# Kernel optimization log

Measured on AMD Instinct MI355X. Metric: run time of the kernel, lower is better.

The kernel has to match this reference:

```python
import jax, jax.numpy as jnp
import numpy as np

NUM_GRAPHS = 1024


def setup_inputs() -> dict:
    key = jax.random.key(0)
    k1, k2, k3, k4, k5, k6 = jax.random.split(key, 6)
    N, F_DIM, E = 100000, 512, 3200000
    x = jax.random.normal(k1, (N, F_DIM), dtype=jnp.float32)
    edge_index = jax.random.randint(k2, (2, E), 0, N, dtype=jnp.int64)
    edge_attr = jax.random.normal(k3, (E, 7), dtype=jnp.float32)
    batch_size = jnp.sort(jax.random.randint(k4, (N,), 0, NUM_GRAPHS, dtype=jnp.int64))
    W = jax.random.normal(k5, (7, F_DIM), dtype=jnp.float32) * 0.02
    b = jax.random.normal(k6, (7,), dtype=jnp.float32) * 0.02
    return {"x": x, "edge_index": edge_index, "edge_attr": edge_attr,
            "batch_size": batch_size, "W": W, "b": b}


def reference(x, edge_index, edge_attr, batch_size, W, b):
    # Faithful to source forward: conv1/conv2 outputs (h) are discarded by the
    # original code; the returned value depends only on x via mean-pool + linear.
    # global_mean_pool over per-node graph ids
    sums = jax.ops.segment_sum(x, batch_size, num_segments=NUM_GRAPHS)  # [G, F]
    counts = jax.ops.segment_sum(jnp.ones((x.shape[0],), dtype=x.dtype),
                                 batch_size, num_segments=NUM_GRAPHS)  # [G]
    pooled = sums / jnp.maximum(counts, 1.0)[:, None]
    # dropout(p=0.5) in eval mode is identity
    return pooled @ W.T + b  # [G, 7]
```

## Files before the change

### kernel.cpp

```cpp
#include <hip/hip_runtime.h>

#define NUM_GRAPHS 1024
#define F_DIM 512


__global__ void zero_ws_kernel(float* __restrict__ A, int n) {
    int i = blockIdx.x * blockDim.x + threadIdx.x;
    if (i < n) A[i] = 0.0f;
}

__device__ __forceinline__ void flush_segment(float (&sa)[8], int seg_len,
                                              int g, int lane,
                                              const float* __restrict__ W,
                                              float* __restrict__ A) {
    const float4* wl = (const float4*)(W + lane * 4);
    #pragma unroll
    for (int j = 0; j < 7; ++j) {
        float4 w0 = wl[j * (F_DIM / 4)];
        float4 w1 = wl[j * (F_DIM / 4) + 64];
        float v = sa[0] * w0.x + sa[1] * w0.y + sa[2] * w0.z + sa[3] * w0.w
                + sa[4] * w1.x + sa[5] * w1.y + sa[6] * w1.z + sa[7] * w1.w;
        #pragma unroll
        for (int off = 32; off > 0; off >>= 1)
            v += __shfl_down(v, off, 64);
        if (lane == 0) atomicAdd(A + g * 8 + j, v);
    }
    if (lane == 0) atomicAdd(A + g * 8 + 7, (float)seg_len);
    #pragma unroll
    for (int k = 0; k < 8; ++k) sa[k] = 0.0f;
}

__global__ __launch_bounds__(256) void node_accum_kernel(
        const float* __restrict__ x, const int* __restrict__ batch,
        const float* __restrict__ W, float* __restrict__ A, int N) {
    const int lane = threadIdx.x & 63;
    const int wave = (blockIdx.x * blockDim.x + threadIdx.x) >> 6;
    const int num_waves = (gridDim.x * blockDim.x) >> 6;
    const int K = (N + num_waves - 1) / num_waves;
    const int start = wave * K;
    const int len = min(N - start, K);
    if (len <= 0) return;

    int g_l = batch[start + min(lane, len - 1)];
    int g_prev = __shfl_up(g_l, 1, 64);
    unsigned long long bnd =
        __ballot(lane > 0 && lane < len && g_l != g_prev);

    const float* xb = x + (size_t)start * F_DIM + lane * 4;

    const float* p1 = xb + (size_t)min(1, len - 1) * F_DIM;
    float4 a0 = ((const float4*)xb)[0];
    float4 c0 = *(const float4*)(xb + F_DIM / 2);
    float4 a1 = ((const float4*)p1)[0];
    float4 c1 = *(const float4*)(p1 + F_DIM / 2);

    float sa[8];
    #pragma unroll
    for (int k = 0; k < 8; ++k) sa[k] = 0.0f;
    int seg_start = 0;
    int g_cur = __shfl(g_l, 0, 64);

    for (int t = 0; t < len; t += 2) {
        const float* p2 = xb + (size_t)min(t + 2, len - 1) * F_DIM;
        float4 n0a = ((const float4*)p2)[0];
        float4 n0c = *(const float4*)(p2 + F_DIM / 2);

        sa[0] += a0.x; sa[1] += a0.y; sa[2] += a0.z; sa[3] += a0.w;
        sa[4] += c0.x; sa[5] += c0.y; sa[6] += c0.z; sa[7] += c0.w;
        if ((t + 1 == len) || ((bnd >> (t + 1)) & 1ULL)) {
            flush_segment(sa, t + 1 - seg_start, g_cur, lane, W, A);
            seg_start = t + 1;
            if (t + 1 < len) g_cur = __shfl(g_l, t + 1, 64);
        }

        const float* p3 = xb + (size_t)min(t + 3, len - 1) * F_DIM;
        float4 n1a = ((const float4*)p3)[0];
        float4 n1c = *(const float4*)(p3 + F_DIM / 2);

        if (t + 1 < len) {
            sa[0] += a1.x; sa[1] += a1.y; sa[2] += a1.z; sa[3] += a1.w;
            sa[4] += c1.x; sa[5] += c1.y; sa[6] += c1.z; sa[7] += c1.w;
            if ((t + 2 == len) || ((bnd >> (t + 2)) & 1ULL)) {
                flush_segment(sa, t + 2 - seg_start, g_cur, lane, W, A);
                seg_start = t + 2;
                if (t + 2 < len) g_cur = __shfl(g_l, t + 2, 64);
            }
        }
        a0 = n0a; c0 = n0c; a1 = n1a; c1 = n1c;
    }
}

__global__ void finalize_kernel(const float* __restrict__ A,
                                const float* __restrict__ b,
                                float* __restrict__ out) {
    int idx = blockIdx.x * blockDim.x + threadIdx.x;
    if (idx >= NUM_GRAPHS * 7) return;
    int g = idx / 7;
    int j = idx - g * 7;
    float cnt = A[g * 8 + 7];
    out[idx] = A[g * 8 + j] / fmaxf(cnt, 1.0f) + b[j];
}

extern "C" void kernel_launch(void* const* d_in, const int* in_sizes, int n_in,
                              void* d_out, int out_size, void* d_ws, size_t ws_size,
                              hipStream_t stream) {
    const float* x     = (const float*)d_in[0];
    const int*   batch = (const int*)d_in[3];
    const float* W     = (const float*)d_in[4];
    const float* b     = (const float*)d_in[5];
    float* out = (float*)d_out;
    float* A   = (float*)d_ws;
    const int N = in_sizes[3];

    const int ws_elems = NUM_GRAPHS * 8;
    zero_ws_kernel<<<(ws_elems + 255) / 256, 256, 0, stream>>>(A, ws_elems);

    node_accum_kernel<<<2048, 256, 0, stream>>>(x, batch, W, A, N);

    finalize_kernel<<<(NUM_GRAPHS * 7 + 255) / 256, 256, 0, stream>>>(A, b, out);
}
```

Baseline: 331.1 us.

## Assign contiguous row chunks per block and interleave rows across its waves

Rows are now split into one contiguous chunk per block, and the 4 waves in a block take rows in a stride-4 interleave, instead of each wave owning its own contiguous chunk. Neighbouring waves therefore read adjacent rows, which is meant to improve DRAM locality. Segment boundaries are detected per row by shuffling graph ids, and the prefetch pipeline is kept two rows deep. The cost is that each wave now flushes every segment its rows touch, so each graph gets up to four times as many atomics and W reads.

Measured after the change: 343.1 us. 1.04x slower.

```diff
diff --git a/kernel.cpp b/kernel.cpp
--- a/kernel.cpp
+++ b/kernel.cpp
@@ -9,7 +9,7 @@
     if (i < n) A[i] = 0.0f;
 }
 
-__device__ __forceinline__ void flush_segment(float (&sa)[8], int seg_len,
+__device__ __forceinline__ void flush_segment(float (&sa)[8], int seg_cnt,
                                               int g, int lane,
                                               const float* __restrict__ W,
                                               float* __restrict__ A) {
@@ -25,7 +25,7 @@
             v += __shfl_down(v, off, 64);
         if (lane == 0) atomicAdd(A + g * 8 + j, v);
     }
-    if (lane == 0) atomicAdd(A + g * 8 + 7, (float)seg_len);
+    if (lane == 0) atomicAdd(A + g * 8 + 7, (float)seg_cnt);
     #pragma unroll
     for (int k = 0; k < 8; ++k) sa[k] = 0.0f;
 }
@@ -34,59 +34,52 @@
         const float* __restrict__ x, const int* __restrict__ batch,
         const float* __restrict__ W, float* __restrict__ A, int N) {
     const int lane = threadIdx.x & 63;
-    const int wave = (blockIdx.x * blockDim.x + threadIdx.x) >> 6;
-    const int num_waves = (gridDim.x * blockDim.x) >> 6;
-    const int K = (N + num_waves - 1) / num_waves;
-    const int start = wave * K;
-    const int len = min(N - start, K);
-    if (len <= 0) return;
+    const int wj   = threadIdx.x >> 6;
+    const int C = (N + gridDim.x - 1) / gridDim.x;
+    const int base = blockIdx.x * C;
+    const int len = min(N - base, C);
+    if (len <= 0 || wj >= len) return;
 
-    int g_l = batch[start + min(lane, len - 1)];
-    int g_prev = __shfl_up(g_l, 1, 64);
-    unsigned long long bnd =
-        __ballot(lane > 0 && lane < len && g_l != g_prev);
+    int g_l = batch[base + min(lane, len - 1)];
 
-    const float* xb = x + (size_t)start * F_DIM + lane * 4;
+    const int T = (len - wj + 3) >> 2;
+    const int rmax = wj + 4 * (T - 1);
 
-    const float* p1 = xb + (size_t)min(1, len - 1) * F_DIM;
-    float4 a0 = ((const float4*)xb)[0];
-    float4 c0 = *(const float4*)(xb + F_DIM / 2);
+    const float* xb = x + (size_t)base * F_DIM + lane * 4;
+
+    const float* p0 = xb + (size_t)wj * F_DIM;
+    const float* p1 = xb + (size_t)min(wj + 4, rmax) * F_DIM;
+    float4 a0 = ((const float4*)p0)[0];
+    float4 c0 = *(const float4*)(p0 + F_DIM / 2);
     float4 a1 = ((const float4*)p1)[0];
     float4 c1 = *(const float4*)(p1 + F_DIM / 2);
 
     float sa[8];
     #pragma unroll
     for (int k = 0; k < 8; ++k) sa[k] = 0.0f;
-    int seg_start = 0;
-    int g_cur = __shfl(g_l, 0, 64);
+    int seg_cnt = 0;
+    int g_cur = __shfl(g_l, wj, 64);
 
-    for (int t = 0; t < len; t += 2) {
-        const float* p2 = xb + (size_t)min(t + 2, len - 1) * F_DIM;
-        float4 n0a = ((const float4*)p2)[0];
-        float4 n0c = *(const float4*)(p2 + F_DIM / 2);
+    for (int t = 0; t < T; ++t) {
+        const int r = wj + 4 * t;
+        const float* p2 = xb + (size_t)min(r + 8, rmax) * F_DIM;
+        float4 na = ((const float4*)p2)[0];
+        float4 nc = *(const float4*)(p2 + F_DIM / 2);
 
         sa[0] += a0.x; sa[1] += a0.y; sa[2] += a0.z; sa[3] += a0.w;
         sa[4] += c0.x; sa[5] += c0.y; sa[6] += c0.z; sa[7] += c0.w;
-        if ((t + 1 == len) || ((bnd >> (t + 1)) & 1ULL)) {
-            flush_segment(sa, t + 1 - seg_start, g_cur, lane, W, A);
-            seg_start = t + 1;
-            if (t + 1 < len) g_cur = __shfl(g_l, t + 1, 64);
+        ++seg_cnt;
+
+        bool last = (r + 4 > rmax);
+        int g_next = g_cur;
+        if (!last) g_next = __shfl(g_l, r + 4, 64);
+        if (last || g_next != g_cur) {
+            flush_segment(sa, seg_cnt, g_cur, lane, W, A);
+            seg_cnt = 0;
+            g_cur = g_next;
         }
 
-        const float* p3 = xb + (size_t)min(t + 3, len - 1) * F_DIM;
-        float4 n1a = ((const float4*)p3)[0];
-        float4 n1c = *(const float4*)(p3 + F_DIM / 2);
-
-        if (t + 1 < len) {
-            sa[0] += a1.x; sa[1] += a1.y; sa[2] += a1.z; sa[3] += a1.w;
-            sa[4] += c1.x; sa[5] += c1.y; sa[6] += c1.z; sa[7] += c1.w;
-            if ((t + 2 == len) || ((bnd >> (t + 2)) & 1ULL)) {
-                flush_segment(sa, t + 2 - seg_start, g_cur, lane, W, A);
-                seg_start = t + 2;
-                if (t + 2 < len) g_cur = __shfl(g_l, t + 2, 64);
-            }
-        }
-        a0 = n0a; c0 = n0c; a1 = n1a; c1 = n1c;
+        a0 = a1; c0 = c1; a1 = na; c1 = nc;
     }
 }
 
```
